# Optimization experiments

Measured on AMD Instinct MI355X. Metric: run time of the kernel, lower is better.

Reference implementation:

```python
import jax, jax.numpy as jnp
import numpy as np
from functools import partial

N = 100000
E = 1600000
F_IN, F_HID, F_OUT = 128, 128, 64


def setup_inputs() -> dict:
    key = jax.random.key(0)
    ks = jax.random.split(key, 10)
    x = jax.random.normal(ks[0], (N, F_IN), dtype=jnp.float32)
    edge_index = jax.random.randint(ks[1], (2, E), 0, N, dtype=jnp.int64)
    edge_attr = jax.random.uniform(ks[2], (E,), dtype=jnp.float32)
    # GCNConv params: Linear(in, out, bias=False) weight + separate bias
    def glorot(k, fan_in, fan_out):
        lim = jnp.sqrt(6.0 / (fan_in + fan_out))
        return jax.random.uniform(k, (fan_in, fan_out), minval=-lim, maxval=lim, dtype=jnp.float32)
    return {
        "x": x, "edge_index": edge_index, "edge_attr": edge_attr,
        "W1": glorot(ks[3], F_IN, F_HID),  "b1": jnp.zeros((F_HID,), jnp.float32),
        "W2": glorot(ks[4], F_HID, F_HID), "b2": jnp.zeros((F_HID,), jnp.float32),
        "W3": glorot(ks[5], F_HID, F_OUT), "b3": jnp.zeros((F_OUT,), jnp.float32),
    }


def _gcn_norm(src, dst, ew, n):
    # PyG gcn_norm: add self-loops with weight 1, symmetric normalization.
    loop = jnp.arange(n, dtype=src.dtype)
    src_f = jnp.concatenate([src, loop])
    dst_f = jnp.concatenate([dst, loop])
    ew_f = jnp.concatenate([ew, jnp.ones((n,), ew.dtype)])
    deg = jax.ops.segment_sum(ew_f, dst_f, num_segments=n)
    dinv = jnp.where(deg > 0, jax.lax.rsqrt(deg), 0.0)
    norm = dinv[src_f] * ew_f * dinv[dst_f]  # [E+N]
    return src_f, dst_f, norm


def _gcn_conv(x, W, b, src_f, dst_f, norm, n):
    h = x @ W  # [N, out]
    msg = norm[:, None] * h[src_f]  # gather + per-edge scale
    out = jax.ops.segment_sum(msg, dst_f, num_segments=n)  # scatter-add
    return out + b


def reference(x, edge_index, edge_attr, W1, b1, W2, b2, W3, b3):
    n = x.shape[0]
    src, dst = edge_index[0], edge_index[1]
    src_f, dst_f, norm = _gcn_norm(src, dst, edge_attr, n)
    h = jax.nn.relu(_gcn_conv(x, W1, b1, src_f, dst_f, norm, n))
    h = jax.nn.relu(_gcn_conv(h, W2, b2, src_f, dst_f, norm, n))
    out = _gcn_conv(h, W3, b3, src_f, dst_f, norm, n)
    return jax.nn.log_softmax(out, axis=-1)
```

## Files before the change

### kernel.cpp

```cpp
#include <hip/hip_runtime.h>

typedef unsigned short ushortT;
typedef unsigned int uintT;
typedef unsigned long long ullT;
typedef __attribute__((ext_vector_type(8))) short bf16x8;
typedef __attribute__((ext_vector_type(4))) float f32x4;

#define NBUCK 391
#define EPB   4096
#define NBEB  391
#define BSLOT 4608

union H16 { ushortT u; _Float16 h; };

__device__ __forceinline__ float bf2f(uintT u16) {
    return __uint_as_float(u16 << 16);
}
__device__ __forceinline__ float bflo(uintT u) {
    return __uint_as_float(u << 16);
}
__device__ __forceinline__ float bfhi(uintT u) {
    return __uint_as_float(u & 0xffff0000u);
}
__device__ __forceinline__ ushortT f2bf(float f) {
    unsigned int u = __float_as_uint(f);
    unsigned int r = (u + 0x7fffu + ((u >> 16) & 1u)) >> 16;
    return (ushortT)r;
}

#define ACC8(U, W) \
    acc[0] = fmaf(W, bflo(U.x), acc[0]); acc[1] = fmaf(W, bfhi(U.x), acc[1]); \
    acc[2] = fmaf(W, bflo(U.y), acc[2]); acc[3] = fmaf(W, bfhi(U.y), acc[3]); \
    acc[4] = fmaf(W, bflo(U.z), acc[4]); acc[5] = fmaf(W, bfhi(U.z), acc[5]); \
    acc[6] = fmaf(W, bflo(U.w), acc[6]); acc[7] = fmaf(W, bfhi(U.w), acc[7]);


__device__ __forceinline__ void twist_body(const float* W, ushortT* Wt, int K, int C, int idx) {
    if (idx < K * C) {
        int k = idx / C, c = idx - k * C;
        Wt[c * K + k] = f2bf(W[idx]);
    }
}

template <int C, bool ABF16>
__device__ __forceinline__ void gemm_body(const void* Aop, const ushortT* Wt,
                                          ushortT* outp, int nrows, int bid, int tid) {
    const int K = 128;
    int wv = tid >> 6;
    int ln = tid & 63;
    int row0 = (bid * 4 + wv) * 16;
    if (row0 >= nrows) return;
    int rA = ln & 15;
    int kg = ln >> 4;
    int rowA = row0 + rA;
    bool okA = rowA < nrows;

    bf16x8 af[4];
    if (ABF16) {
        const ushortT* A = (const ushortT*)Aop;
        #pragma unroll
        for (int kb = 0; kb < 4; ++kb) {
            if (okA) af[kb] = *(const bf16x8*)(A + (size_t)rowA * K + kb * 32 + kg * 8);
            else     af[kb] = (bf16x8)(short)0;
        }
    } else {
        const float* A = (const float*)Aop;
        #pragma unroll
        for (int kb = 0; kb < 4; ++kb) {
            bf16x8 t = (bf16x8)(short)0;
            if (okA) {
                const float4* ap = reinterpret_cast<const float4*>(A + (size_t)rowA * K + kb * 32 + kg * 8);
                float4 p0 = ap[0], p1 = ap[1];
                t[0] = (short)f2bf(p0.x); t[1] = (short)f2bf(p0.y);
                t[2] = (short)f2bf(p0.z); t[3] = (short)f2bf(p0.w);
                t[4] = (short)f2bf(p1.x); t[5] = (short)f2bf(p1.y);
                t[6] = (short)f2bf(p1.z); t[7] = (short)f2bf(p1.w);
            }
            af[kb] = t;
        }
    }

    int colB = ln & 15;
    f32x4 acc[C / 16];
    #pragma unroll
    for (int nt = 0; nt < C / 16; ++nt) acc[nt] = (f32x4)0.0f;
    #pragma unroll
    for (int nt = 0; nt < C / 16; ++nt) {
        int c = nt * 16 + colB;
        #pragma unroll
        for (int kb = 0; kb < 4; ++kb) {
            bf16x8 bfr = *(const bf16x8*)(Wt + c * K + kb * 32 + kg * 8);
            acc[nt] = __builtin_amdgcn_mfma_f32_16x16x32_bf16(af[kb], bfr, acc[nt], 0, 0, 0);
        }
    }
    #pragma unroll
    for (int nt = 0; nt < C / 16; ++nt) {
        #pragma unroll
        for (int r = 0; r < 4; ++r) {
            int rowC = row0 + (ln >> 4) * 4 + r;
            if (rowC < nrows) outp[(size_t)rowC * C + nt * 16 + colB] = f2bf(acc[nt][r]);
        }
    }
}

__global__ __launch_bounds__(512) void k_sort_twist(const int* src, const int* dst, const float* ew,
                                                    int* bucket_count, ullT* erec, int e,
                                                    const float* W1, ushortT* Wt1,
                                                    const float* W2, ushortT* Wt2,
                                                    const float* W3, ushortT* Wt3) {
    __shared__ ullT srec[EPB];
    __shared__ int  gaddr[EPB];
    __shared__ int  hist[512];
    __shared__ int  adj[NBUCK];
    int blk = blockIdx.x, t = threadIdx.x;
    if (blk >= NBEB) {
        int tb = blk - NBEB;
        if (tb < 32)      twist_body(W1, Wt1, 128, 128, tb * 512 + t);
        else if (tb < 64) twist_body(W2, Wt2, 128, 128, (tb - 32) * 512 + t);
        else              twist_body(W3, Wt3, 128, 64, (tb - 64) * 512 + t);
        return;
    }
    hist[t] = 0;
    __syncthreads();
    int base = blk * EPB;
    for (int j = t; j < EPB; j += 512) {
        int i = base + j;
        if (i < e) atomicAdd(&hist[dst[i] >> 8], 1);
    }
    __syncthreads();
    int myc = hist[t];
    for (int off = 1; off < 512; off <<= 1) {
        int x = 0; if (t >= off) x = hist[t - off];
        __syncthreads();
        if (t >= off) hist[t] += x;
        __syncthreads();
    }
    int lb = (t == 0) ? 0 : hist[t - 1];
    __syncthreads();
    hist[t] = lb;
    if (t < NBUCK) {
        int gb = 0;
        if (myc > 0) gb = atomicAdd(&bucket_count[t], myc);
        adj[t] = t * BSLOT + gb - lb;
    }
    __syncthreads();
    for (int j = t; j < EPB; j += 512) {
        int i = base + j;
        if (i < e) {
            int d = dst[i];
            int b = d >> 8;
            int pos = atomicAdd(&hist[b], 1);
            H16 cv; cv.h = (_Float16)ew[i];
            ullT rec = ((ullT)(uintT)src[i] << 24) | ((ullT)(uintT)(d & 255) << 16) | (ullT)cv.u;
            srec[pos] = rec;
            int ga = adj[b] + pos;
            int lim = b * BSLOT + BSLOT - 1;
            gaddr[pos] = ga <= lim ? ga : lim;
        }
    }
    __syncthreads();
    int m = e - base; if (m > EPB) m = EPB;
    for (int k = t; k < m; k += 512) {
        erec[(size_t)gaddr[k]] = srec[k];
    }
}

__global__ __launch_bounds__(256) void k_bucket_gemm1(const ullT* erec,
                                                      const int* bucket_count,
                                                      uintT* entries, float* dinv, int* counts, int n,
                                                      const float* x, const ushortT* Wt1,
                                                      ushortT* hw1) {
    __shared__ int cnt[256];
    __shared__ uintT wsum[256];
    int blk = blockIdx.x, t = threadIdx.x;
    if (blk < NBUCK) {
        int b = blk;
        cnt[t] = 0; wsum[t] = 0;
        __syncthreads();
        int beg = b * BSLOT, m = bucket_count[b];
        if (m > BSLOT) m = BSLOT;
        for (int j = t; j < m; j += 256) {
            ullT rec = erec[(size_t)beg + j];
            int dlow = (int)((rec >> 16) & 255);
            ushortT hu = (ushortT)(rec & 0xffffu);
            int slot = atomicAdd(&cnt[dlow], 1);
            H16 cv; cv.u = hu;
            atomicAdd(&wsum[dlow], (uintT)__float2uint_rn((float)cv.h * 16777216.0f));
            if (slot < 64) {
                uintT s = (uintT)(rec >> 24);
                entries[((size_t)b * 256 + dlow) * 64 + slot] = (s << 15) | (uintT)hu;
            }
        }
        __syncthreads();
        int node = b * 256 + t;
        if (node < n) {
            float sum = (float)wsum[t] * (1.0f / 16777216.0f);
            dinv[node] = rsqrtf(1.0f + sum);
            int c = cnt[t];
            counts[node] = c > 64 ? 64 : c;
        }
    } else {
        gemm_body<128, false>(x, Wt1, hw1, n, blk - NBUCK, t);
    }
}

template <int C>
__global__ __launch_bounds__(1024) void k_agg_gemm(const char* hwb, const float* dinv,
                                                   const int* counts, const uintT* entries,
                                                   const float* bias, const ushortT* Wt,
                                                   ushortT* outp, int n) {
    __shared__ ullT wp[16][64];
    __shared__ uintT rows[16][64];
    int wv = threadIdx.x >> 6, ln = threadIdx.x & 63;
    int i = blockIdx.x * 16 + wv;
    int lg = ln & 15;
    int gp = ln >> 4;

    float wfac = dinv[i];
    int cnt = counts[i];
    int cntp = (cnt + 7) & ~7;
    uintT ent = entries[(size_t)i * 64 + ln];
    int s_l = (ln < cnt) ? (int)(ent >> 15) : 0;
    H16 cv; cv.u = (ushortT)(ent & 0x7fffu);
    float w_l = (ln < cnt) ? dinv[s_l] * (float)cv.h * wfac : 0.f;
    wp[wv][ln] = ((ullT)__float_as_uint(w_l) << 32) | (ullT)((uintT)s_l << 8);
    const ullT* wpw = wp[wv];

    const char* lane_base = hwb + (size_t)(lg * 16);
    uint4 uself = *(const uint4*)(lane_base + (size_t)i * 256);

    float acc[8];
    #pragma unroll
    for (int j = 0; j < 8; ++j) acc[j] = 0.f;

    ullT pa = wpw[gp], pb = wpw[4 + gp];
    uint4 ua = *(const uint4*)(lane_base + (uintT)pa);
    uint4 ub = *(const uint4*)(lane_base + (uintT)pb);
    for (int e = 8; e < cntp; e += 8) {
        ullT pa2 = wpw[e + gp], pb2 = wpw[e + 4 + gp];
        uint4 ua2 = *(const uint4*)(lane_base + (uintT)pa2);
        uint4 ub2 = *(const uint4*)(lane_base + (uintT)pb2);
        float wa = __uint_as_float((uintT)(pa >> 32));
        float wb = __uint_as_float((uintT)(pb >> 32));
        ACC8(ua, wa)
        ACC8(ub, wb)
        pa = pa2; pb = pb2; ua = ua2; ub = ub2;
    }
    {
        float wa = __uint_as_float((uintT)(pa >> 32));
        float wb = __uint_as_float((uintT)(pb >> 32));
        ACC8(ua, wa)
        ACC8(ub, wb)
    }

    #pragma unroll
    for (int j = 0; j < 8; ++j) {
        acc[j] += __shfl_xor(acc[j], 16);
        acc[j] += __shfl_xor(acc[j], 32);
    }
    float selfw = wfac * wfac;
    ACC8(uself, selfw)

    float a0 = (gp & 1) ? ((gp & 2) ? acc[6] : acc[2]) : ((gp & 2) ? acc[4] : acc[0]);
    float a1 = (gp & 1) ? ((gp & 2) ? acc[7] : acc[3]) : ((gp & 2) ? acc[5] : acc[1]);
    int d = lg * 4 + gp;
    float2 bs = *(const float2*)(bias + 2 * d);
    a0 = fmaxf(a0 + bs.x, 0.f);
    a1 = fmaxf(a1 + bs.y, 0.f);
    uintT packed = (uintT)f2bf(a0) | ((uintT)f2bf(a1) << 16);
    rows[wv][((d * 4) ^ ((wv & 7) << 4)) >> 2] = packed;
    __syncthreads();

    if (wv < C / 16) {
        int nt = wv;
        int rA = ln & 15;
        int kg = ln >> 4;
        int colB = ln & 15;
        const char* rbase = (const char*)&rows[0][0];
        bf16x8 af[4];
        #pragma unroll
        for (int kb = 0; kb < 4; ++kb) {
            int byteoff = (kb * 64 + kg * 16) ^ ((rA & 7) << 4);
            af[kb] = *(const bf16x8*)(rbase + rA * 256 + byteoff);
        }
        f32x4 gac = (f32x4)0.0f;
        int c = nt * 16 + colB;
        #pragma unroll
        for (int kb = 0; kb < 4; ++kb) {
            bf16x8 bfr = *(const bf16x8*)(Wt + c * 128 + kb * 32 + kg * 8);
            gac = __builtin_amdgcn_mfma_f32_16x16x32_bf16(af[kb], bfr, gac, 0, 0, 0);
        }
        int row0 = blockIdx.x * 16;
        #pragma unroll
        for (int r = 0; r < 4; ++r) {
            int rowC = row0 + kg * 4 + r;
            outp[(size_t)rowC * C + nt * 16 + colB] = f2bf(gac[r]);
        }
    }
}

__global__ __launch_bounds__(256) void k_agg_softmax(const char* hwb, const float* dinv,
                                                     const int* counts, const uintT* entries,
                                                     const float* bias, float* outp, int n) {
    __shared__ ullT wp[4][64];
    int wv = threadIdx.x >> 6, ln = threadIdx.x & 63;
    int i = blockIdx.x * 4 + wv;
    if (i >= n) return;
    int lg = ln & 7;
    int gp = ln >> 3;

    float wfac = dinv[i];
    int cnt = counts[i];
    int cntp = (cnt + 7) & ~7;
    uintT ent = entries[(size_t)i * 64 + ln];
    int s_l = (ln < cnt) ? (int)(ent >> 15) : 0;
    H16 cv; cv.u = (ushortT)(ent & 0x7fffu);
    float w_l = (ln < cnt) ? dinv[s_l] * (float)cv.h * wfac : 0.f;
    wp[wv][ln] = ((ullT)__float_as_uint(w_l) << 32) | (ullT)((uintT)s_l << 7);
    const ullT* wpw = wp[wv];

    const char* lane_base = hwb + (size_t)(lg * 16);
    uint4 uself = *(const uint4*)(lane_base + (size_t)i * 128);

    float acc[8];
    #pragma unroll
    for (int j = 0; j < 8; ++j) acc[j] = 0.f;

    ullT pa = wpw[gp];
    uint4 ua = *(const uint4*)(lane_base + (uintT)pa);
    for (int e = 8; e < cntp; e += 8) {
        ullT pa2 = wpw[e + gp];
        uint4 ua2 = *(const uint4*)(lane_base + (uintT)pa2);
        float wa = __uint_as_float((uintT)(pa >> 32));
        ACC8(ua, wa)
        pa = pa2; ua = ua2;
    }
    {
        float wa = __uint_as_float((uintT)(pa >> 32));
        ACC8(ua, wa)
    }

    #pragma unroll
    for (int j = 0; j < 8; ++j) {
        acc[j] += __shfl_xor(acc[j], 8);
        acc[j] += __shfl_xor(acc[j], 16);
        acc[j] += __shfl_xor(acc[j], 32);
    }
    float selfw = wfac * wfac;
    ACC8(uself, selfw)

    float4 bsa = *(const float4*)(bias + lg * 8);
    float4 bsb = *(const float4*)(bias + lg * 8 + 4);
    acc[0] += bsa.x; acc[1] += bsa.y; acc[2] += bsa.z; acc[3] += bsa.w;
    acc[4] += bsb.x; acc[5] += bsb.y; acc[6] += bsb.z; acc[7] += bsb.w;

    float m = acc[0];
    #pragma unroll
    for (int j = 1; j < 8; ++j) m = fmaxf(m, acc[j]);
    m = fmaxf(m, __shfl_xor(m, 1));
    m = fmaxf(m, __shfl_xor(m, 2));
    m = fmaxf(m, __shfl_xor(m, 4));
    float s = 0.f;
    #pragma unroll
    for (int j = 0; j < 8; ++j) s += __expf(acc[j] - m);
    s += __shfl_xor(s, 1);
    s += __shfl_xor(s, 2);
    s += __shfl_xor(s, 4);
    float ls = m + __logf(s);

    float v0 = (gp & 1) ? acc[4] : acc[0];
    float v1 = (gp & 1) ? acc[5] : acc[1];
    float v2 = (gp & 1) ? acc[6] : acc[2];
    float v3 = (gp & 1) ? acc[7] : acc[3];
    if (gp < 2) {
        float4 r = { v0 - ls, v1 - ls, v2 - ls, v3 - ls };
        *(float4*)(outp + (size_t)i * 64 + lg * 8 + gp * 4) = r;
    }
}

extern "C" void kernel_launch(void* const* d_in, const int* in_sizes, int n_in,
                              void* d_out, int out_size, void* d_ws, size_t ws_size,
                              hipStream_t stream) {
    const int N = 100000, E = 1600000;
    const int NPAD = NBUCK * 256;
    const float* x  = (const float*)d_in[0];
    const int*   src = (const int*)d_in[1];
    const int*   dst = src + E;
    const float* ea = (const float*)d_in[2];
    const float* W1 = (const float*)d_in[3];
    const float* b1 = (const float*)d_in[4];
    const float* W2 = (const float*)d_in[5];
    const float* b2 = (const float*)d_in[6];
    const float* W3 = (const float*)d_in[7];
    const float* b3 = (const float*)d_in[8];
    float* outp = (float*)d_out;

    char* ws = (char*)d_ws;
    auto alloc = [&](size_t bytes) {
        char* p = ws;
        ws += (bytes + 255) & ~(size_t)255;
        return p;
    };
    int*   bucket_count = (int*)alloc((size_t)NBUCK * 4);
    ullT*  erec         = (ullT*)alloc((size_t)NBUCK * BSLOT * 8);
    float* dinv    = (float*)alloc((size_t)N * 4);
    int*   counts  = (int*)  alloc((size_t)N * 4);
    uintT* entries = (uintT*)alloc((size_t)NPAD * 64 * 4);
    ushortT* Wt1   = (ushortT*)alloc(128 * 128 * 2);
    ushortT* Wt2   = (ushortT*)alloc(128 * 128 * 2);
    ushortT* Wt3   = (ushortT*)alloc(128 * 64 * 2);
    ushortT* hwA   = (ushortT*)alloc((size_t)N * 128 * 2);
    ushortT* hwB   = (ushortT*)alloc((size_t)N * 128 * 2);

    const int nbGemm = (N + 63) / 64;
    const int nbFused = N / 16;
    const int nbAgg  = (N + 3) / 4;

    hipMemsetAsync(bucket_count, 0, (size_t)NBUCK * 4, stream);
    k_sort_twist<<<NBEB + 80, 512, 0, stream>>>(src, dst, ea, bucket_count, erec, E,
                                                W1, Wt1, W2, Wt2, W3, Wt3);
    k_bucket_gemm1<<<NBUCK + nbGemm, 256, 0, stream>>>(erec, bucket_count,
                                                       entries, dinv, counts, N,
                                                       x, Wt1, hwA);
    k_agg_gemm<128><<<nbFused, 1024, 0, stream>>>((const char*)hwA, dinv, counts, entries,
                                                  b1, Wt2, hwB, N);
    k_agg_gemm<64><<<nbFused, 1024, 0, stream>>>((const char*)hwB, dinv, counts, entries,
                                                 b2, Wt3, hwA, N);
    k_agg_softmax<<<nbAgg, 256, 0, stream>>>((const char*)hwA, dinv, counts, entries,
                                             b3, outp, N);
}
```

Measured before the change: 370.7 us.

## Process four nodes per wave in fused aggregate-GEMM with 256-thread blocks

The fused aggregation+GEMM kernel drops from 1024-thread blocks (one node per wave) to 256-thread blocks where each wave aggregates four nodes in sequence. All four nodes' metadata and source dinv values are loaded up front, and every wave then takes part in the MFMA stage by covering C/64 column tiles. The aim is to make the block-wide barrier and MFMA stage cheaper and to keep all waves busy in the GEMM. In exchange, each wave works through its nodes serially, so there is less parallelism for hiding gather latency. Padded lanes now use a zero offset.

New measurement: 363.8 us. About the same (-1.9%).

```diff
diff --git a/kernel.cpp b/kernel.cpp
--- a/kernel.cpp
+++ b/kernel.cpp
@@ -205,74 +205,92 @@
 }
 
 template <int C>
-__global__ __launch_bounds__(1024) void k_agg_gemm(const char* hwb, const float* dinv,
-                                                   const int* counts, const uintT* entries,
-                                                   const float* bias, const ushortT* Wt,
-                                                   ushortT* outp, int n) {
-    __shared__ ullT wp[16][64];
+__global__ __launch_bounds__(256) void k_agg_gemm(const char* hwb, const float* dinv,
+                                                  const int* counts, const uintT* entries,
+                                                  const float* bias, const ushortT* Wt,
+                                                  ushortT* outp, int n) {
+    __shared__ ullT wp[4][64];
     __shared__ uintT rows[16][64];
     int wv = threadIdx.x >> 6, ln = threadIdx.x & 63;
-    int i = blockIdx.x * 16 + wv;
+    int tile0 = blockIdx.x * 16;
     int lg = ln & 15;
     int gp = ln >> 4;
 
-    float wfac = dinv[i];
-    int cnt = counts[i];
-    int cntp = (cnt + 7) & ~7;
-    uintT ent = entries[(size_t)i * 64 + ln];
-    int s_l = (ln < cnt) ? (int)(ent >> 15) : 0;
-    H16 cv; cv.u = (ushortT)(ent & 0x7fffu);
-    float w_l = (ln < cnt) ? dinv[s_l] * (float)cv.h * wfac : 0.f;
-    wp[wv][ln] = ((ullT)__float_as_uint(w_l) << 32) | (ullT)((uintT)s_l << 8);
-    const ullT* wpw = wp[wv];
+    float wfac4[4], wsrc4[4];
+    int   cnt4[4];
+    uintT ent4[4];
+    #pragma unroll
+    for (int nn = 0; nn < 4; ++nn) {
+        int i = tile0 + wv * 4 + nn;
+        wfac4[nn] = dinv[i];
+        cnt4[nn]  = counts[i];
+        ent4[nn]  = entries[(size_t)i * 64 + ln];
+        wsrc4[nn] = dinv[(int)(ent4[nn] >> 15)];
+    }
 
     const char* lane_base = hwb + (size_t)(lg * 16);
-    uint4 uself = *(const uint4*)(lane_base + (size_t)i * 256);
-
-    float acc[8];
-    #pragma unroll
-    for (int j = 0; j < 8; ++j) acc[j] = 0.f;
-
-    ullT pa = wpw[gp], pb = wpw[4 + gp];
-    uint4 ua = *(const uint4*)(lane_base + (uintT)pa);
-    uint4 ub = *(const uint4*)(lane_base + (uintT)pb);
-    for (int e = 8; e < cntp; e += 8) {
-        ullT pa2 = wpw[e + gp], pb2 = wpw[e + 4 + gp];
-        uint4 ua2 = *(const uint4*)(lane_base + (uintT)pa2);
-        uint4 ub2 = *(const uint4*)(lane_base + (uintT)pb2);
-        float wa = __uint_as_float((uintT)(pa >> 32));
-        float wb = __uint_as_float((uintT)(pb >> 32));
-        ACC8(ua, wa)
-        ACC8(ub, wb)
-        pa = pa2; pb = pb2; ua = ua2; ub = ub2;
-    }
+
+    #pragma unroll
+    for (int nn = 0; nn < 4; ++nn) {
+        int r = wv * 4 + nn;
+        int i = tile0 + r;
+        float wfac = wfac4[nn];
+        int cnt = cnt4[nn];
+        int cntp = (cnt + 7) & ~7;
+        uintT ent = ent4[nn];
+        int s_l = (ln < cnt) ? (int)(ent >> 15) : 0;
+        H16 cv; cv.u = (ushortT)(ent & 0x7fffu);
+        float w_l = (ln < cnt) ? wsrc4[nn] * (float)cv.h * wfac : 0.f;
+        uintT soff = (ln < cnt) ? ((uintT)s_l << 8) : 0u;
+        wp[wv][ln] = ((ullT)__float_as_uint(w_l) << 32) | (ullT)soff;
+        const ullT* wpw = wp[wv];
+
+        uint4 uself = *(const uint4*)(lane_base + (size_t)i * 256);
+
+        float acc[8];
+        #pragma unroll
+        for (int j = 0; j < 8; ++j) acc[j] = 0.f;
+
+        ullT pa = wpw[gp], pb = wpw[4 + gp];
+        uint4 ua = *(const uint4*)(lane_base + (uintT)pa);
+        uint4 ub = *(const uint4*)(lane_base + (uintT)pb);
+        for (int e = 8; e < cntp; e += 8) {
+            ullT pa2 = wpw[e + gp], pb2 = wpw[e + 4 + gp];
+            uint4 ua2 = *(const uint4*)(lane_base + (uintT)pa2);
+            uint4 ub2 = *(const uint4*)(lane_base + (uintT)pb2);
+            float wa = __uint_as_float((uintT)(pa >> 32));
+            float wb = __uint_as_float((uintT)(pb >> 32));
+            ACC8(ua, wa)
+            ACC8(ub, wb)
+            pa = pa2; pb = pb2; ua = ua2; ub = ub2;
+        }
+        {
+            float wa = __uint_as_float((uintT)(pa >> 32));
+            float wb = __uint_as_float((uintT)(pb >> 32));
+            ACC8(ua, wa)
+            ACC8(ub, wb)
+        }
+
+        #pragma unroll
+        for (int j = 0; j < 8; ++j) {
+            acc[j] += __shfl_xor(acc[j], 16);
+            acc[j] += __shfl_xor(acc[j], 32);
+        }
+        float selfw = wfac * wfac;
+        ACC8(uself, selfw)
+
+        float a0 = (gp & 1) ? ((gp & 2) ? acc[6] : acc[2]) : ((gp & 2) ? acc[4] : acc[0]);
+        float a1 = (gp & 1) ? ((gp & 2) ? acc[7] : acc[3]) : ((gp & 2) ? acc[5] : acc[1]);
+        int d = lg * 4 + gp;
+        float2 bs = *(const float2*)(bias + 2 * d);
+        a0 = fmaxf(a0 + bs.x, 0.f);
+        a1 = fmaxf(a1 + bs.y, 0.f);
+        uintT packed = (uintT)f2bf(a0) | ((uintT)f2bf(a1) << 16);
+        rows[r][((d * 4) ^ ((r & 7) << 4)) >> 2] = packed;
+    }
+    __syncthreads();
+
     {
-        float wa = __uint_as_float((uintT)(pa >> 32));
-        float wb = __uint_as_float((uintT)(pb >> 32));
-        ACC8(ua, wa)
-        ACC8(ub, wb)
-    }
-
-    #pragma unroll
-    for (int j = 0; j < 8; ++j) {
-        acc[j] += __shfl_xor(acc[j], 16);
-        acc[j] += __shfl_xor(acc[j], 32);
-    }
-    float selfw = wfac * wfac;
-    ACC8(uself, selfw)
-
-    float a0 = (gp & 1) ? ((gp & 2) ? acc[6] : acc[2]) : ((gp & 2) ? acc[4] : acc[0]);
-    float a1 = (gp & 1) ? ((gp & 2) ? acc[7] : acc[3]) : ((gp & 2) ? acc[5] : acc[1]);
-    int d = lg * 4 + gp;
-    float2 bs = *(const float2*)(bias + 2 * d);
-    a0 = fmaxf(a0 + bs.x, 0.f);
-    a1 = fmaxf(a1 + bs.y, 0.f);
-    uintT packed = (uintT)f2bf(a0) | ((uintT)f2bf(a1) << 16);
-    rows[wv][((d * 4) ^ ((wv & 7) << 4)) >> 2] = packed;
-    __syncthreads();
-
-    if (wv < C / 16) {
-        int nt = wv;
         int rA = ln & 15;
         int kg = ln >> 4;
         int colB = ln & 15;
@@ -283,18 +301,22 @@
             int byteoff = (kb * 64 + kg * 16) ^ ((rA & 7) << 4);
             af[kb] = *(const bf16x8*)(rbase + rA * 256 + byteoff);
         }
-        f32x4 gac = (f32x4)0.0f;
-        int c = nt * 16 + colB;
-        #pragma unroll
-        for (int kb = 0; kb < 4; ++kb) {
-            bf16x8 bfr = *(const bf16x8*)(Wt + c * 128 + kb * 32 + kg * 8);
-            gac = __builtin_amdgcn_mfma_f32_16x16x32_bf16(af[kb], bfr, gac, 0, 0, 0);
-        }
-        int row0 = blockIdx.x * 16;
-        #pragma unroll
-        for (int r = 0; r < 4; ++r) {
-            int rowC = row0 + kg * 4 + r;
-            outp[(size_t)rowC * C + nt * 16 + colB] = f2bf(gac[r]);
+        const int NS = C / 64;
+        #pragma unroll
+        for (int s = 0; s < NS; ++s) {
+            int nt = wv * NS + s;
+            f32x4 gac = (f32x4)0.0f;
+            int c = nt * 16 + colB;
+            #pragma unroll
+            for (int kb = 0; kb < 4; ++kb) {
+                bf16x8 bfr = *(const bf16x8*)(Wt + c * 128 + kb * 32 + kg * 8);
+                gac = __builtin_amdgcn_mfma_f32_16x16x32_bf16(af[kb], bfr, gac, 0, 0, 0);
+            }
+            #pragma unroll
+            for (int r = 0; r < 4; ++r) {
+                int rowC = tile0 + kg * 4 + r;
+                outp[(size_t)rowC * C + nt * 16 + colB] = f2bf(gac[r]);
+            }
         }
     }
 }
@@ -422,10 +444,10 @@
     k_bucket_gemm1<<<NBUCK + nbGemm, 256, 0, stream>>>(erec, bucket_count,
                                                        entries, dinv, counts, N,
                                                        x, Wt1, hwA);
-    k_agg_gemm<128><<<nbFused, 1024, 0, stream>>>((const char*)hwA, dinv, counts, entries,
-                                                  b1, Wt2, hwB, N);
-    k_agg_gemm<64><<<nbFused, 1024, 0, stream>>>((const char*)hwB, dinv, counts, entries,
-                                                 b2, Wt3, hwA, N);
+    k_agg_gemm<128><<<nbFused, 256, 0, stream>>>((const char*)hwA, dinv, counts, entries,
+                                                 b1, Wt2, hwB, N);
+    k_agg_gemm<64><<<nbFused, 256, 0, stream>>>((const char*)hwB, dinv, counts, entries,
+                                                b2, Wt3, hwA, N);
     k_agg_softmax<<<nbAgg, 256, 0, stream>>>((const char*)hwA, dinv, counts, entries,
                                              b3, outp, N);
 }
```

## Run fused aggregate-GEMM with one wavefront per 16-node tile

Applied to the files above, without the earlier changes.

The fused aggregation+GEMM kernel changes from 1024-thread blocks, with one wave per node, to 64-thread blocks where a single wave loops over all 16 nodes of a tile. It prefetches the next node's edge entries and source dinv while working on the current one, then runs every MFMA column tile itself. This removes the block-wide barrier where most waves sat idle during the GEMM phase and allows finer-grained scheduling. The cost is serialized per-wave work: gather latency for each node now depends on in-wave prefetch and on occupancy across many small blocks, rather than 16 concurrent waves per block.

After: 370.5 us. Within noise of the previous version (-0.0%).

```diff
diff --git a/kernel.cpp b/kernel.cpp
--- a/kernel.cpp
+++ b/kernel.cpp
@@ -205,74 +205,88 @@
 }
 
 template <int C>
-__global__ __launch_bounds__(1024) void k_agg_gemm(const char* hwb, const float* dinv,
-                                                   const int* counts, const uintT* entries,
-                                                   const float* bias, const ushortT* Wt,
-                                                   ushortT* outp, int n) {
-    __shared__ ullT wp[16][64];
+__global__ __launch_bounds__(64) void k_agg_gemm(const char* hwb, const float* dinv,
+                                                 const int* counts, const uintT* entries,
+                                                 const float* bias, const ushortT* Wt,
+                                                 ushortT* outp, int n) {
+    __shared__ ullT wp[64];
     __shared__ uintT rows[16][64];
-    int wv = threadIdx.x >> 6, ln = threadIdx.x & 63;
-    int i = blockIdx.x * 16 + wv;
+    int ln = threadIdx.x;
+    int tile0 = blockIdx.x * 16;
     int lg = ln & 15;
     int gp = ln >> 4;
 
-    float wfac = dinv[i];
-    int cnt = counts[i];
-    int cntp = (cnt + 7) & ~7;
-    uintT ent = entries[(size_t)i * 64 + ln];
-    int s_l = (ln < cnt) ? (int)(ent >> 15) : 0;
-    H16 cv; cv.u = (ushortT)(ent & 0x7fffu);
-    float w_l = (ln < cnt) ? dinv[s_l] * (float)cv.h * wfac : 0.f;
-    wp[wv][ln] = ((ullT)__float_as_uint(w_l) << 32) | (ullT)((uintT)s_l << 8);
-    const ullT* wpw = wp[wv];
-
     const char* lane_base = hwb + (size_t)(lg * 16);
-    uint4 uself = *(const uint4*)(lane_base + (size_t)i * 256);
-
-    float acc[8];
-    #pragma unroll
-    for (int j = 0; j < 8; ++j) acc[j] = 0.f;
-
-    ullT pa = wpw[gp], pb = wpw[4 + gp];
-    uint4 ua = *(const uint4*)(lane_base + (uintT)pa);
-    uint4 ub = *(const uint4*)(lane_base + (uintT)pb);
-    for (int e = 8; e < cntp; e += 8) {
-        ullT pa2 = wpw[e + gp], pb2 = wpw[e + 4 + gp];
-        uint4 ua2 = *(const uint4*)(lane_base + (uintT)pa2);
-        uint4 ub2 = *(const uint4*)(lane_base + (uintT)pb2);
-        float wa = __uint_as_float((uintT)(pa >> 32));
-        float wb = __uint_as_float((uintT)(pb >> 32));
-        ACC8(ua, wa)
-        ACC8(ub, wb)
-        pa = pa2; pb = pb2; ua = ua2; ub = ub2;
-    }
+    float2 bs = *(const float2*)(bias + 2 * (lg * 4 + gp));
+
+    float wfac_n = dinv[tile0];
+    int   cnt_n  = counts[tile0];
+    uintT ent_n  = entries[(size_t)tile0 * 64 + ln];
+    float wsrc_n = dinv[(int)(ent_n >> 15)];
+
+    #pragma unroll 1
+    for (int nn = 0; nn < 16; ++nn) {
+        int i = tile0 + nn;
+        float wfac = wfac_n;
+        int cnt = cnt_n;
+        uintT ent = ent_n;
+        float wsrc = wsrc_n;
+        if (nn < 15) {
+            wfac_n = dinv[i + 1];
+            cnt_n  = counts[i + 1];
+            ent_n  = entries[(size_t)(i + 1) * 64 + ln];
+            wsrc_n = dinv[(int)(ent_n >> 15)];
+        }
+        int cntp = (cnt + 7) & ~7;
+        H16 cv; cv.u = (ushortT)(ent & 0x7fffu);
+        float w_l = (ln < cnt) ? wsrc * (float)cv.h * wfac : 0.f;
+        uintT soff = (ln < cnt) ? ((ent >> 15) << 8) : 0u;
+        wp[ln] = ((ullT)__float_as_uint(w_l) << 32) | (ullT)soff;
+
+        uint4 uself = *(const uint4*)(lane_base + (size_t)i * 256);
+
+        float acc[8];
+        #pragma unroll
+        for (int j = 0; j < 8; ++j) acc[j] = 0.f;
+
+        ullT pa = wp[gp], pb = wp[4 + gp];
+        uint4 ua = *(const uint4*)(lane_base + (uintT)pa);
+        uint4 ub = *(const uint4*)(lane_base + (uintT)pb);
+        for (int e = 8; e < cntp; e += 8) {
+            ullT pa2 = wp[e + gp], pb2 = wp[e + 4 + gp];
+            uint4 ua2 = *(const uint4*)(lane_base + (uintT)pa2);
+            uint4 ub2 = *(const uint4*)(lane_base + (uintT)pb2);
+            float wa = __uint_as_float((uintT)(pa >> 32));
+            float wb = __uint_as_float((uintT)(pb >> 32));
+            ACC8(ua, wa)
+            ACC8(ub, wb)
+            pa = pa2; pb = pb2; ua = ua2; ub = ub2;
+        }
+        {
+            float wa = __uint_as_float((uintT)(pa >> 32));
+            float wb = __uint_as_float((uintT)(pb >> 32));
+            ACC8(ua, wa)
+            ACC8(ub, wb)
+        }
+
+        #pragma unroll
+        for (int j = 0; j < 8; ++j) {
+            acc[j] += __shfl_xor(acc[j], 16);
+            acc[j] += __shfl_xor(acc[j], 32);
+        }
+        float selfw = wfac * wfac;
+        ACC8(uself, selfw)
+
+        float a0 = (gp & 1) ? ((gp & 2) ? acc[6] : acc[2]) : ((gp & 2) ? acc[4] : acc[0]);
+        float a1 = (gp & 1) ? ((gp & 2) ? acc[7] : acc[3]) : ((gp & 2) ? acc[5] : acc[1]);
+        a0 = fmaxf(a0 + bs.x, 0.f);
+        a1 = fmaxf(a1 + bs.y, 0.f);
+        uintT packed = (uintT)f2bf(a0) | ((uintT)f2bf(a1) << 16);
+        rows[nn][(((lg * 4 + gp) * 4) ^ ((nn & 7) << 4)) >> 2] = packed;
+    }
+    __syncthreads();
+
     {
-        float wa = __uint_as_float((uintT)(pa >> 32));
-        float wb = __uint_as_float((uintT)(pb >> 32));
-        ACC8(ua, wa)
-        ACC8(ub, wb)
-    }
-
-    #pragma unroll
-    for (int j = 0; j < 8; ++j) {
-        acc[j] += __shfl_xor(acc[j], 16);
-        acc[j] += __shfl_xor(acc[j], 32);
-    }
-    float selfw = wfac * wfac;
-    ACC8(uself, selfw)
-
-    float a0 = (gp & 1) ? ((gp & 2) ? acc[6] : acc[2]) : ((gp & 2) ? acc[4] : acc[0]);
-    float a1 = (gp & 1) ? ((gp & 2) ? acc[7] : acc[3]) : ((gp & 2) ? acc[5] : acc[1]);
-    int d = lg * 4 + gp;
-    float2 bs = *(const float2*)(bias + 2 * d);
-    a0 = fmaxf(a0 + bs.x, 0.f);
-    a1 = fmaxf(a1 + bs.y, 0.f);
-    uintT packed = (uintT)f2bf(a0) | ((uintT)f2bf(a1) << 16);
-    rows[wv][((d * 4) ^ ((wv & 7) << 4)) >> 2] = packed;
-    __syncthreads();
-
-    if (wv < C / 16) {
-        int nt = wv;
         int rA = ln & 15;
         int kg = ln >> 4;
         int colB = ln & 15;
@@ -283,18 +297,20 @@
             int byteoff = (kb * 64 + kg * 16) ^ ((rA & 7) << 4);
             af[kb] = *(const bf16x8*)(rbase + rA * 256 + byteoff);
         }
-        f32x4 gac = (f32x4)0.0f;
-        int c = nt * 16 + colB;
-        #pragma unroll
-        for (int kb = 0; kb < 4; ++kb) {
-            bf16x8 bfr = *(const bf16x8*)(Wt + c * 128 + kb * 32 + kg * 8);
-            gac = __builtin_amdgcn_mfma_f32_16x16x32_bf16(af[kb], bfr, gac, 0, 0, 0);
-        }
-        int row0 = blockIdx.x * 16;
-        #pragma unroll
-        for (int r = 0; r < 4; ++r) {
-            int rowC = row0 + kg * 4 + r;
-            outp[(size_t)rowC * C + nt * 16 + colB] = f2bf(gac[r]);
+        #pragma unroll
+        for (int nt = 0; nt < C / 16; ++nt) {
+            f32x4 gac = (f32x4)0.0f;
+            int c = nt * 16 + colB;
+            #pragma unroll
+            for (int kb = 0; kb < 4; ++kb) {
+                bf16x8 bfr = *(const bf16x8*)(Wt + c * 128 + kb * 32 + kg * 8);
+                gac = __builtin_amdgcn_mfma_f32_16x16x32_bf16(af[kb], bfr, gac, 0, 0, 0);
+            }
+            #pragma unroll
+            for (int r = 0; r < 4; ++r) {
+                int rowC = tile0 + kg * 4 + r;
+                outp[(size_t)rowC * C + nt * 16 + colB] = f2bf(gac[r]);
+            }
         }
     }
 }
@@ -422,10 +438,10 @@
     k_bucket_gemm1<<<NBUCK + nbGemm, 256, 0, stream>>>(erec, bucket_count,
                                                        entries, dinv, counts, N,
                                                        x, Wt1, hwA);
-    k_agg_gemm<128><<<nbFused, 1024, 0, stream>>>((const char*)hwA, dinv, counts, entries,
-                                                  b1, Wt2, hwB, N);
-    k_agg_gemm<64><<<nbFused, 1024, 0, stream>>>((const char*)hwB, dinv, counts, entries,
-                                                 b2, Wt3, hwA, N);
+    k_agg_gemm<128><<<nbFused, 64, 0, stream>>>((const char*)hwA, dinv, counts, entries,
+                                                b1, Wt2, hwB, N);
+    k_agg_gemm<64><<<nbFused, 64, 0, stream>>>((const char*)hwB, dinv, counts, entries,
+                                               b2, Wt3, hwA, N);
     k_agg_softmax<<<nbAgg, 256, 0, stream>>>((const char*)hwA, dinv, counts, entries,
                                              b3, outp, N);
 }
```
